# Performance work log

Measured on AMD Instinct MI355X. Metric: run time of the kernel, lower is better.

The kernel has to match this reference:

```python
import jax, jax.numpy as jnp
import numpy as np

IMG_SIZE = np.array([960.0, 512.0], np.float32)   # network input size (w, h)
HM_SIZE = np.array([480.0, 256.0], np.float32)    # heatmap size = IMG_SIZE / 2 (w, h)
GRID_SIZE = np.array([8000.0, 8000.0, 2000.0], np.float32)  # mm
CUBE = (80, 80, 20)
NBINS = CUBE[0] * CUBE[1] * CUBE[2]


def _base_grid():
    # linspace(-size/2, size/2, nbins) per axis, meshgrid indexing='ij' (torch default)
    axes = [np.linspace(-GRID_SIZE[d] / 2, GRID_SIZE[d] / 2, CUBE[d], dtype=np.float32) for d in range(3)]
    gx, gy, gz = np.meshgrid(*axes, indexing='ij')
    return jnp.asarray(np.stack([gx.ravel(), gy.ravel(), gz.ravel()], axis=1))  # [NBINS, 3]


def _bilinear_sample(img, coords):
    # img: [C,H,W]; coords: [P,2] normalized to [-1,1], align_corners=True, zero padding
    C, H, W = img.shape
    ix = (coords[:, 0] + 1.0) * 0.5 * (W - 1)
    iy = (coords[:, 1] + 1.0) * 0.5 * (H - 1)
    x0 = jnp.floor(ix)
    y0 = jnp.floor(iy)
    x1 = x0 + 1.0
    y1 = y0 + 1.0
    wx1 = ix - x0
    wx0 = 1.0 - wx1
    wy1 = iy - y0
    wy0 = 1.0 - wy1

    def corner(xi, yi, w):
        valid = (xi >= 0) & (xi <= W - 1) & (yi >= 0) & (yi <= H - 1)
        xc = jnp.clip(xi, 0, W - 1).astype(jnp.int32)
        yc = jnp.clip(yi, 0, H - 1).astype(jnp.int32)
        vals = img[:, yc, xc]  # [C,P]
        return vals * (w * valid.astype(img.dtype))[None, :]

    return (corner(x0, y0, wx0 * wy0) + corner(x1, y0, wx1 * wy0)
            + corner(x0, y1, wx0 * wy1) + corner(x1, y1, wx1 * wy1))  # [C,P]


def reference(heatmaps, R, T, f, c_cam, trans, wh, grid_center):
    # heatmaps: [N,B,C,H,W]; R:[N,B,3,3]; T:[N,B,3]; f,c_cam,wh:[N,B,2]; trans:[N,B,2,3]; grid_center:[B,3]
    N, B, C, H, W = heatmaps.shape
    hm = jnp.asarray(HM_SIZE)
    img_sz = jnp.asarray(IMG_SIZE)

    grids = _base_grid()[None, :, :] + grid_center[:, None, :]          # [B,P,3]
    pts = grids[None, :, :, :] - T[:, :, None, :]                        # [N,B,P,3]
    xcam = jnp.einsum('nbij,nbpj->nbpi', R, pts)                         # [N,B,P,3]
    xy = f[:, :, None, :] * (xcam[..., :2] / xcam[..., 2:3]) + c_cam[:, :, None, :]  # pixel coords

    bnd = jnp.all((xy >= 0) & (xy < wh[:, :, None, :]), axis=-1).astype(heatmaps.dtype)  # [N,B,P]

    mx = jnp.max(wh, axis=-1)[:, :, None, None]
    xy = jnp.minimum(jnp.maximum(xy, -1.0), mx)
    xy1 = jnp.concatenate([xy, jnp.ones_like(xy[..., :1])], axis=-1)     # homogeneous
    xy = jnp.einsum('nbij,nbpj->nbpi', trans, xy1)                       # affine to network image space
    xy = xy * (hm / img_sz)
    sg = jnp.clip(xy / (hm - 1.0) * 2.0 - 1.0, -1.1, 1.1)                # [N,B,P,2]

    samples = jax.vmap(_bilinear_sample)(
        heatmaps.reshape(N * B, C, H, W), sg.reshape(N * B, NBINS, 2)
    ).reshape(N, B, C, NBINS)                                            # [N,B,C,P]

    bnd_e = bnd[:, :, None, :]                                           # [N,B,1,P]
    cubes = jnp.sum(samples * bnd_e, axis=0) / (jnp.sum(bnd_e, axis=0) + 1e-6)  # [B,C,P]
    cubes = jnp.nan_to_num(cubes)
    cubes = jnp.clip(cubes, 0.0, 1.0)  # feature_op = False
    cubes = cubes.reshape(B, C, CUBE[0], CUBE[1], CUBE[2])
    return cubes, grids


def setup_inputs():
    key = jax.random.key(0)
    k_hm, k_gc = jax.random.split(key)
    N, B, C, H, W = 5, 8, 15, 256, 480
    heatmaps = jax.random.uniform(k_hm, (N, B, C, H, W), jnp.float32)

    # plausible look-at cameras around the space center
    center = np.array([0.0, -500.0, 800.0], np.float32)
    Rs, Ts = [], []
    for i in range(N):
        ang = 2.0 * np.pi * i / N
        pos = center + np.array([6000.0 * np.cos(ang), 6000.0 * np.sin(ang), 1200.0], np.float32)
        fwd = center - pos
        fwd = fwd / np.linalg.norm(fwd)
        up = np.array([0.0, 0.0, 1.0], np.float32)
        right = np.cross(fwd, up)
        right = right / np.linalg.norm(right)
        down = np.cross(fwd, right)
        Rs.append(np.stack([right, down, fwd]).astype(np.float32))
        Ts.append(pos)
    R = jnp.asarray(np.broadcast_to(np.stack(Rs)[:, None], (N, B, 3, 3)).copy())
    T = jnp.asarray(np.broadcast_to(np.stack(Ts)[:, None], (N, B, 3)).copy())
    f = jnp.full((N, B, 2), 1500.0, jnp.float32)
    wh_np = np.array([1920.0, 1080.0], np.float32)  # original image width/height
    c_cam = jnp.asarray(np.broadcast_to(wh_np / 2, (N, B, 2)).copy())
    s = IMG_SIZE / wh_np
    tr = np.array([[s[0], 0.0, 0.0], [0.0, s[1], 0.0]], np.float32)
    trans = jnp.asarray(np.broadcast_to(tr, (N, B, 2, 3)).copy())
    wh = jnp.asarray(np.broadcast_to(wh_np, (N, B, 2)).copy())
    grid_center = jnp.asarray(center)[None, :] + 200.0 * jax.random.normal(k_gc, (B, 3), jnp.float32)
    return dict(heatmaps=heatmaps, R=R, T=T, f=f, c_cam=c_cam, trans=trans, wh=wh, grid_center=grid_center)
```

## Files before the change

kernel.cpp:

```cpp
#include <hip/hip_runtime.h>
#include <stdint.h>

#define N_VIEWS 5
#define B_ 8
#define C_ 15
#define CP_ 16
#define H_ 256
#define W_ 480
#define NBINS 128000
#define HW_ (H_ * W_)
#define CUBES_ELEMS (B_ * C_ * NBINS)
#define NB_ (N_VIEWS * B_)

typedef float v2f __attribute__((ext_vector_type(2)));

__global__ __launch_bounds__(256) void transpose_fp8_kernel(
    const float* __restrict__ hm, uint32_t* __restrict__ tp)
{
    const int bid  = blockIdx.x;
    const int b    = bid & 7;
    const int rest = bid >> 3;
    const int n    = rest % 5;
    const int tile = rest / 5;
    const int cb   = n * B_ + b;
    const int idx  = tile * 256 + (int)threadIdx.x;
    if (idx >= HW_) return;
    const float* src = hm + (size_t)cb * C_ * HW_ + idx;
    float v[CP_];
#pragma unroll
    for (int c = 0; c < C_; ++c) v[c] = src[(size_t)c * HW_];
    v[15] = 0.0f;
    uint32_t w[4];
#pragma unroll
    for (int j = 0; j < 4; ++j) {
        int r = 0;
        r = __builtin_amdgcn_cvt_pk_fp8_f32(v[4*j + 0], v[4*j + 1], r, false);
        r = __builtin_amdgcn_cvt_pk_fp8_f32(v[4*j + 2], v[4*j + 3], r, true);
        w[j] = (uint32_t)r;
    }
    uint4* dst = (uint4*)(tp + ((size_t)cb * HW_ + (size_t)idx) * 4);
    *dst = make_uint4(w[0], w[1], w[2], w[3]);
}

struct Proj { int o00, o10, o01, o11; float w00, w10, w01, w11, inb; };

__device__ __forceinline__ Proj project_one(
    int cb, float gx, float gy, float gz,
    const float* __restrict__ R, const float* __restrict__ T,
    const float* __restrict__ f, const float* __restrict__ ccam,
    const float* __restrict__ trans, const float* __restrict__ wh)
{
    Proj r;
    const float* Rn = R + cb * 9;
    const float px = gx - T[cb * 3 + 0];
    const float py = gy - T[cb * 3 + 1];
    const float pz = gz - T[cb * 3 + 2];
    const float xcm = Rn[0] * px + Rn[1] * py + Rn[2] * pz;
    const float ycm = Rn[3] * px + Rn[4] * py + Rn[5] * pz;
    const float zcm = Rn[6] * px + Rn[7] * py + Rn[8] * pz;
    const float u = f[cb * 2 + 0] * (xcm / zcm) + ccam[cb * 2 + 0];
    const float v = f[cb * 2 + 1] * (ycm / zcm) + ccam[cb * 2 + 1];
    const float w0 = wh[cb * 2 + 0], w1 = wh[cb * 2 + 1];
    const bool inb = (u >= 0.0f) & (u < w0) & (v >= 0.0f) & (v < w1);
    const float inbf = inb ? 1.0f : 0.0f;
    const float mx = fmaxf(w0, w1);
    const float uu = fminf(fmaxf(u, -1.0f), mx);
    const float vv = fminf(fmaxf(v, -1.0f), mx);
    const float* tr = trans + cb * 6;
    const float tx = (tr[0] * uu + tr[1] * vv + tr[2]) * 0.5f;
    const float ty = (tr[3] * uu + tr[4] * vv + tr[5]) * 0.5f;
    const float sgx = fminf(fmaxf(tx / 479.0f * 2.0f - 1.0f, -1.1f), 1.1f);
    const float sgy = fminf(fmaxf(ty / 255.0f * 2.0f - 1.0f, -1.1f), 1.1f);
    const float ixf = (sgx + 1.0f) * 0.5f * 479.0f;
    const float iyf = (sgy + 1.0f) * 0.5f * 255.0f;
    const float x0 = floorf(ixf), y0 = floorf(iyf);
    const float x1 = x0 + 1.0f, y1 = y0 + 1.0f;
    const float wx1 = ixf - x0, wy1 = iyf - y0;
    const float wx0 = 1.0f - wx1, wy0 = 1.0f - wy1;
    const float v00 = (x0 >= 0.0f && y0 >= 0.0f) ? inbf : 0.0f;
    const float v10 = (x1 <= 479.0f && y0 >= 0.0f) ? inbf : 0.0f;
    const float v01 = (x0 >= 0.0f && y1 <= 255.0f) ? inbf : 0.0f;
    const float v11 = (x1 <= 479.0f && y1 <= 255.0f) ? inbf : 0.0f;
    r.w00 = wx0 * wy0 * v00; r.w10 = wx1 * wy0 * v10;
    r.w01 = wx0 * wy1 * v01; r.w11 = wx1 * wy1 * v11;
    const int xi0 = min(max((int)x0, 0), W_ - 1);
    const int yi0 = min(max((int)y0, 0), H_ - 1);
    const int xi1 = min(max((int)x1, 0), W_ - 1);
    const int yi1 = min(max((int)y1, 0), H_ - 1);
    const int o00 = yi0 * W_ + xi0, o10 = yi0 * W_ + xi1;
    const int o01 = yi1 * W_ + xi0, o11 = yi1 * W_ + xi1;
    r.o00 = inb ? o00 : 0; r.o10 = inb ? o10 : 0;
    r.o01 = inb ? o01 : 0; r.o11 = inb ? o11 : 0;
    r.inb = inbf;
    return r;
}

__device__ __forceinline__ void acc_pixel(float* acc, uint4 q, float wgt)
{
    const uint32_t u[4] = { q.x, q.y, q.z, q.w };
#pragma unroll
    for (int j = 0; j < 4; ++j) {
        v2f lo = __builtin_amdgcn_cvt_pk_f32_fp8(u[j], false);
        v2f hi = __builtin_amdgcn_cvt_pk_f32_fp8(u[j], true);
        acc[4*j + 0] += wgt * lo.x;
        acc[4*j + 1] += wgt * lo.y;
        acc[4*j + 2] += wgt * hi.x;
        acc[4*j + 3] += wgt * hi.y;
    }
}

__global__ __launch_bounds__(256) void project_kernel_fp8(
    const uint32_t* __restrict__ tp,
    const float* __restrict__ R, const float* __restrict__ T,
    const float* __restrict__ f, const float* __restrict__ ccam,
    const float* __restrict__ trans, const float* __restrict__ wh,
    const float* __restrict__ gc,
    float* __restrict__ out)
{
    const int bid  = blockIdx.x;
    const int b    = bid & 7;
    const int tile = bid >> 3;
    const int tz = tile % 5;
    const int ty = (tile / 5) % 10;
    const int tx = tile / 50;
    const int tid = (int)threadIdx.x;
    const int lz = tid & 3;
    const int ly = (tid >> 2) & 7;
    const int lx = tid >> 5;
    const int ixg = tx * 8 + lx;
    const int iyg = ty * 8 + ly;
    const int izg = tz * 4 + lz;
    const int p   = ixg * 1600 + iyg * 20 + izg;

    const float gx = (float)(-4000.0 + ixg * (8000.0 / 79.0)) + gc[b * 3 + 0];
    const float gy = (float)(-4000.0 + iyg * (8000.0 / 79.0)) + gc[b * 3 + 1];
    const float gz = (float)(-1000.0 + izg * (2000.0 / 19.0)) + gc[b * 3 + 2];
    {
        const size_t goff = (size_t)CUBES_ELEMS + ((size_t)b * NBINS + (size_t)p) * 3;
        out[goff + 0] = gx; out[goff + 1] = gy; out[goff + 2] = gz;
    }

    Proj pr[N_VIEWS];
    uint4 q[N_VIEWS][4];
#pragma unroll
    for (int n = 0; n < N_VIEWS; ++n) {
        const int cb = n * B_ + b;
        pr[n] = project_one(cb, gx, gy, gz, R, T, f, ccam, trans, wh);
        const uint4* base = (const uint4*)tp + (size_t)cb * HW_;
        q[n][0] = base[pr[n].o00];
        q[n][1] = base[pr[n].o10];
        q[n][2] = base[pr[n].o01];
        q[n][3] = base[pr[n].o11];
    }

    float acc[CP_];
#pragma unroll
    for (int c = 0; c < CP_; ++c) acc[c] = 0.0f;
    float bndsum = 0.0f;
#pragma unroll
    for (int n = 0; n < N_VIEWS; ++n) {
        bndsum += pr[n].inb;
        acc_pixel(acc, q[n][0], pr[n].w00);
        acc_pixel(acc, q[n][1], pr[n].w10);
        acc_pixel(acc, q[n][2], pr[n].w01);
        acc_pixel(acc, q[n][3], pr[n].w11);
    }

    const float inv = 1.0f / (bndsum + 1e-6f);
    const size_t ob = (size_t)b * C_ * NBINS + (size_t)p;
#pragma unroll
    for (int c = 0; c < C_; ++c) {
        float r = acc[c] * inv;
        r = fmaxf(r, 0.0f);
        r = fminf(r, 1.0f);
        out[ob + (size_t)c * NBINS] = r;
    }
}

__device__ __forceinline__ void decode_grid(int p, int b, const float* __restrict__ gc,
                                            float& gx, float& gy, float& gz)
{
    const int ixg = p / 1600;
    const int rem = p - ixg * 1600;
    const int iyg = rem / 20;
    const int izg = rem - iyg * 20;
    gx = (float)(-4000.0 + ixg * (8000.0 / 79.0)) + gc[b * 3 + 0];
    gy = (float)(-4000.0 + iyg * (8000.0 / 79.0)) + gc[b * 3 + 1];
    gz = (float)(-1000.0 + izg * (2000.0 / 19.0)) + gc[b * 3 + 2];
}

__global__ __launch_bounds__(256) void project_kernel_direct(
    const float* __restrict__ hm,
    const float* __restrict__ R, const float* __restrict__ T,
    const float* __restrict__ f, const float* __restrict__ ccam,
    const float* __restrict__ trans, const float* __restrict__ wh,
    const float* __restrict__ gc,
    float* __restrict__ out)
{
    const int p = blockIdx.x * blockDim.x + threadIdx.x;
    const int b = blockIdx.y;
    if (p >= NBINS) return;
    float gx, gy, gz;
    decode_grid(p, b, gc, gx, gy, gz);
    {
        const size_t goff = (size_t)CUBES_ELEMS + ((size_t)b * NBINS + (size_t)p) * 3;
        out[goff + 0] = gx; out[goff + 1] = gy; out[goff + 2] = gz;
    }
    float acc[C_];
#pragma unroll
    for (int c = 0; c < C_; ++c) acc[c] = 0.0f;
    float bndsum = 0.0f;
#pragma unroll
    for (int n = 0; n < N_VIEWS; ++n) {
        const int cb = n * B_ + b;
        Proj cr = project_one(cb, gx, gy, gz, R, T, f, ccam, trans, wh);
        bndsum += cr.inb;
        const float* img = hm + (size_t)cb * C_ * HW_;
#pragma unroll
        for (int c = 0; c < C_; ++c) {
            const float* ic = img + (size_t)c * HW_;
            acc[c] += cr.w00 * ic[cr.o00] + cr.w10 * ic[cr.o10]
                    + cr.w01 * ic[cr.o01] + cr.w11 * ic[cr.o11];
        }
    }
    const float inv = 1.0f / (bndsum + 1e-6f);
    const size_t ob = (size_t)b * C_ * NBINS + (size_t)p;
#pragma unroll
    for (int c = 0; c < C_; ++c) {
        float r = acc[c] * inv;
        r = fmaxf(r, 0.0f);
        r = fminf(r, 1.0f);
        out[ob + (size_t)c * NBINS] = r;
    }
}

extern "C" void kernel_launch(void* const* d_in, const int* in_sizes, int n_in,
                              void* d_out, int out_size, void* d_ws, size_t ws_size,
                              hipStream_t stream) {
    const float* hm    = (const float*)d_in[0];
    const float* R     = (const float*)d_in[1];
    const float* T     = (const float*)d_in[2];
    const float* f     = (const float*)d_in[3];
    const float* ccam  = (const float*)d_in[4];
    const float* trans = (const float*)d_in[5];
    const float* wh    = (const float*)d_in[6];
    const float* gc    = (const float*)d_in[7];
    float* out = (float*)d_out;

    const size_t ws_needed = (size_t)NB_ * HW_ * CP_;

    if (ws_size >= ws_needed) {
        uint32_t* tp = (uint32_t*)d_ws;
        dim3 tgrid((HW_ / 256) * NB_);
        transpose_fp8_kernel<<<tgrid, 256, 0, stream>>>(hm, tp);
        dim3 grid((NBINS / 256) * B_);
        project_kernel_fp8<<<grid, 256, 0, stream>>>(tp, R, T, f, ccam, trans, wh, gc, out);
    } else {
        dim3 grid(NBINS / 256, B_);
        project_kernel_direct<<<grid, 256, 0, stream>>>(hm, R, T, f, ccam, trans, wh, gc, out);
    }
}
```

Baseline: 502.6 us.

## Stage per-block bounding-box heatmap patch in LDS before bilinear gathers

Each block reduces the pixel bounding box its voxels touch in each view, cooperatively copies that patch of the fp8-packed heatmap into shared memory, and then gathers the four bilinear corners from LDS instead of global memory. If the box exceeds the LDS capacity it falls back to direct global loads. This targets redundant scattered global gathers. In exchange it adds block-wide reductions, several barriers per view and a serialized view loop, which removes the earlier overlap of all views' loads.

```diff
diff --git a/kernel.cpp b/kernel.cpp
--- a/kernel.cpp
+++ b/kernel.cpp
@@ -11,6 +11,7 @@
 #define HW_ (H_ * W_)
 #define CUBES_ELEMS (B_ * C_ * NBINS)
 #define NB_ (N_VIEWS * B_)
+#define LDS_RECS 3072
 
 typedef float v2f __attribute__((ext_vector_type(2)));
 
@@ -42,7 +43,7 @@
     *dst = make_uint4(w[0], w[1], w[2], w[3]);
 }
 
-struct Proj { int o00, o10, o01, o11; float w00, w10, w01, w11, inb; };
+struct Proj { int xi0, yi0, xi1, yi1; float w00, w10, w01, w11, inb; };
 
 __device__ __forceinline__ Proj project_one(
     int cb, float gx, float gy, float gz,
@@ -83,14 +84,10 @@
     const float v11 = (x1 <= 479.0f && y1 <= 255.0f) ? inbf : 0.0f;
     r.w00 = wx0 * wy0 * v00; r.w10 = wx1 * wy0 * v10;
     r.w01 = wx0 * wy1 * v01; r.w11 = wx1 * wy1 * v11;
-    const int xi0 = min(max((int)x0, 0), W_ - 1);
-    const int yi0 = min(max((int)y0, 0), H_ - 1);
-    const int xi1 = min(max((int)x1, 0), W_ - 1);
-    const int yi1 = min(max((int)y1, 0), H_ - 1);
-    const int o00 = yi0 * W_ + xi0, o10 = yi0 * W_ + xi1;
-    const int o01 = yi1 * W_ + xi0, o11 = yi1 * W_ + xi1;
-    r.o00 = inb ? o00 : 0; r.o10 = inb ? o10 : 0;
-    r.o01 = inb ? o01 : 0; r.o11 = inb ? o11 : 0;
+    r.xi0 = min(max((int)x0, 0), W_ - 1);
+    r.yi0 = min(max((int)y0, 0), H_ - 1);
+    r.xi1 = min(max((int)x1, 0), W_ - 1);
+    r.yi1 = min(max((int)y1, 0), H_ - 1);
     r.inb = inbf;
     return r;
 }
@@ -117,6 +114,9 @@
     const float* __restrict__ gc,
     float* __restrict__ out)
 {
+    __shared__ uint4 s_img[LDS_RECS];
+    __shared__ int   s_red[16];
+
     const int bid  = blockIdx.x;
     const int b    = bid & 7;
     const int tile = bid >> 3;
@@ -141,29 +141,77 @@
     }
 
     Proj pr[N_VIEWS];
-    uint4 q[N_VIEWS][4];
-#pragma unroll
-    for (int n = 0; n < N_VIEWS; ++n) {
-        const int cb = n * B_ + b;
-        pr[n] = project_one(cb, gx, gy, gz, R, T, f, ccam, trans, wh);
-        const uint4* base = (const uint4*)tp + (size_t)cb * HW_;
-        q[n][0] = base[pr[n].o00];
-        q[n][1] = base[pr[n].o10];
-        q[n][2] = base[pr[n].o01];
-        q[n][3] = base[pr[n].o11];
-    }
+#pragma unroll
+    for (int n = 0; n < N_VIEWS; ++n)
+        pr[n] = project_one(n * B_ + b, gx, gy, gz, R, T, f, ccam, trans, wh);
 
     float acc[CP_];
 #pragma unroll
     for (int c = 0; c < CP_; ++c) acc[c] = 0.0f;
     float bndsum = 0.0f;
-#pragma unroll
+
+#pragma unroll 1
     for (int n = 0; n < N_VIEWS; ++n) {
-        bndsum += pr[n].inb;
-        acc_pixel(acc, q[n][0], pr[n].w00);
-        acc_pixel(acc, q[n][1], pr[n].w10);
-        acc_pixel(acc, q[n][2], pr[n].w01);
-        acc_pixel(acc, q[n][3], pr[n].w11);
+        const Proj P = pr[n];
+        const bool inb = (P.inb != 0.0f);
+        const uint4* base = (const uint4*)tp + (size_t)(n * B_ + b) * HW_;
+
+        int mnx = inb ? P.xi0 : 0x7fffffff;
+        int mxx = inb ? P.xi1 : (int)0x80000000;
+        int mny = inb ? P.yi0 : 0x7fffffff;
+        int mxy = inb ? P.yi1 : (int)0x80000000;
+#pragma unroll
+        for (int o = 32; o > 0; o >>= 1) {
+            mnx = min(mnx, __shfl_xor(mnx, o));
+            mxx = max(mxx, __shfl_xor(mxx, o));
+            mny = min(mny, __shfl_xor(mny, o));
+            mxy = max(mxy, __shfl_xor(mxy, o));
+        }
+        if ((tid & 63) == 0) {
+            const int wid = tid >> 6;
+            s_red[wid * 4 + 0] = mnx; s_red[wid * 4 + 1] = mxx;
+            s_red[wid * 4 + 2] = mny; s_red[wid * 4 + 3] = mxy;
+        }
+        __syncthreads();
+        mnx = s_red[0]; mxx = s_red[1]; mny = s_red[2]; mxy = s_red[3];
+#pragma unroll
+        for (int w = 1; w < 4; ++w) {
+            mnx = min(mnx, s_red[w * 4 + 0]); mxx = max(mxx, s_red[w * 4 + 1]);
+            mny = min(mny, s_red[w * 4 + 2]); mxy = max(mxy, s_red[w * 4 + 3]);
+        }
+        __syncthreads();
+
+        bndsum += P.inb;
+        if (mnx > mxx) continue;
+
+        const int bw = mxx - mnx + 1;
+        const int bh = mxy - mny + 1;
+        uint4 q00, q10, q01, q11;
+        if (bw * bh <= LDS_RECS) {
+            const int wid = tid >> 6, lane = tid & 63;
+            for (int row = wid; row < bh; row += 4) {
+                const uint4* srow = base + (size_t)(mny + row) * W_ + mnx;
+                uint4* drow = s_img + row * bw;
+                for (int col = lane; col < bw; col += 64) drow[col] = srow[col];
+            }
+            __syncthreads();
+            const int l00 = inb ? (P.yi0 - mny) * bw + (P.xi0 - mnx) : 0;
+            const int l10 = inb ? (P.yi0 - mny) * bw + (P.xi1 - mnx) : 0;
+            const int l01 = inb ? (P.yi1 - mny) * bw + (P.xi0 - mnx) : 0;
+            const int l11 = inb ? (P.yi1 - mny) * bw + (P.xi1 - mnx) : 0;
+            q00 = s_img[l00]; q10 = s_img[l10];
+            q01 = s_img[l01]; q11 = s_img[l11];
+            __syncthreads();
+        } else {
+            q00 = base[inb ? P.yi0 * W_ + P.xi0 : 0];
+            q10 = base[inb ? P.yi0 * W_ + P.xi1 : 0];
+            q01 = base[inb ? P.yi1 * W_ + P.xi0 : 0];
+            q11 = base[inb ? P.yi1 * W_ + P.xi1 : 0];
+        }
+        acc_pixel(acc, q00, P.w00);
+        acc_pixel(acc, q10, P.w10);
+        acc_pixel(acc, q01, P.w01);
+        acc_pixel(acc, q11, P.w11);
     }
 
     const float inv = 1.0f / (bndsum + 1e-6f);
@@ -215,12 +263,17 @@
         const int cb = n * B_ + b;
         Proj cr = project_one(cb, gx, gy, gz, R, T, f, ccam, trans, wh);
         bndsum += cr.inb;
+        const bool inb = (cr.inb != 0.0f);
+        const int o00 = inb ? cr.yi0 * W_ + cr.xi0 : 0;
+        const int o10 = inb ? cr.yi0 * W_ + cr.xi1 : 0;
+        const int o01 = inb ? cr.yi1 * W_ + cr.xi0 : 0;
+        const int o11 = inb ? cr.yi1 * W_ + cr.xi1 : 0;
         const float* img = hm + (size_t)cb * C_ * HW_;
 #pragma unroll
         for (int c = 0; c < C_; ++c) {
             const float* ic = img + (size_t)c * HW_;
-            acc[c] += cr.w00 * ic[cr.o00] + cr.w10 * ic[cr.o10]
-                    + cr.w01 * ic[cr.o01] + cr.w11 * ic[cr.o11];
+            acc[c] += cr.w00 * ic[o00] + cr.w10 * ic[o10]
+                    + cr.w01 * ic[o01] + cr.w11 * ic[o11];
         }
     }
     const float inv = 1.0f / (bndsum + 1e-6f);
```

Result: slower. 586.9 us (+16.8%).
